# Optimization experiments

Hardware: AMD Instinct MI355X
Metric: run time of the kernel (lower is better)

## Reference

```python
import jax, jax.numpy as jnp
import numpy as np

K = 128           # top-k
NUM_SAMPLES = 500 # perturbation samples
SIGMA = 0.05      # noise scale (forward arg sigma in the torch module)


def setup_inputs() -> dict:
    key = jax.random.key(0)
    k1, k2 = jax.random.split(key)
    x = jax.random.normal(k1, (32, 2048), dtype=jnp.float32)
    noise = jax.random.normal(k2, (32, NUM_SAMPLES, 2048), dtype=jnp.float32)
    return {"x": x, "noise": noise}


def reference(x, noise):
    # x: (b, d) scores; noise: (b, n, d) standard-normal perturbations.
    b, d = x.shape
    n = noise.shape[1]
    perturbed = x[:, None, :] + noise * SIGMA          # (b, n, d)
    _, idx = jax.lax.top_k(perturbed, K)               # (b, n, K) indices into d
    idx = jnp.sort(idx, axis=-1)                       # sorted, matching torch.sort
    # indicators[b,j,d] = mean_n one_hot(idx[b,n,j], d)
    # Computed with a scatter-add instead of materializing the (b,n,K,d) one-hot.
    bi = jnp.arange(b)[:, None, None]                  # (b,1,1)
    ki = jnp.arange(K)[None, None, :]                  # (1,1,K)
    counts = jnp.zeros((b, K, d), dtype=x.dtype).at[bi, ki, idx].add(1.0)
    indicators = counts / n                            # (b, K, d)
    return indicators, idx
```

## Files before the change

### kernel.cpp

```cpp
#include <hip/hip_runtime.h>


constexpr int B_     = 32;
constexpr int D_     = 2048;
constexpr int NS_    = 500;
constexpr int TOPK_  = 128;
constexpr int SLACK_ = 32;
constexpr float SIGMA_  = 0.05f;
constexpr int PER_LANE_ = D_ / 64;
constexpr int HALF_  = D_ / 2;
constexpr int HPL_   = HALF_ / 64;
constexpr int CAP_   = 256;
constexpr int SLOTS_ = CAP_ / 64;
constexpr int JCHUNK_ = 8;

__device__ __forceinline__ uint32_t order_key(float f) {
  uint32_t u = __float_as_uint(f);
  return (u & 0x80000000u) ? ~u : (u | 0x80000000u);
}
__device__ __forceinline__ float inv_key(uint32_t k) {
  uint32_t u = (k & 0x80000000u) ? (k & 0x7FFFFFFFu) : ~k;
  return __uint_as_float(u);
}

__global__ __launch_bounds__(64) void ptk_cutoff(const float* __restrict__ x,
                                                 float* __restrict__ cutf) {
  const int lane = threadIdx.x & 63;
  const int b = blockIdx.x;
  const float* __restrict__ xr = x + (size_t)b * D_;
  uint32_t keys[PER_LANE_];
#pragma unroll
  for (int j = 0; j < PER_LANE_; j += 4) {
    const float4 xv = *reinterpret_cast<const float4*>(xr + lane * PER_LANE_ + j);
    keys[j + 0] = order_key(xv.x); keys[j + 1] = order_key(xv.y);
    keys[j + 2] = order_key(xv.z); keys[j + 3] = order_key(xv.w);
  }
  uint32_t prefix = 0; int k = TOPK_ + SLACK_;
#pragma unroll 1
  for (int bit = 31; bit >= 0; --bit) {
    const uint32_t want = (prefix >> bit) | 1u;
    int c = 0;
#pragma unroll
    for (int j = 0; j < PER_LANE_; ++j) c += ((keys[j] >> bit) == want) ? 1 : 0;
#pragma unroll
    for (int off = 32; off >= 1; off >>= 1) c += __shfl_xor(c, off);
    if (c >= k) prefix |= (1u << bit); else k -= c;
  }
  if (lane == 0) cutf[b] = inv_key(prefix);
}

__global__ __launch_bounds__(256) void ptk_select(
    const float* __restrict__ x, const float* __restrict__ noise,
    const float* __restrict__ cutf, float* __restrict__ out_idx) {
  __shared__ uint2 comp[2][2 * CAP_];
  __shared__ int cnts[2][2];

  const int lane = threadIdx.x & 63;
  const int wave = threadIdx.x >> 6;
  const int pair = wave >> 1;
  const int half = wave & 1;
  const int row  = blockIdx.x * 2 + pair;
  const int b = row / NS_;

  const float* __restrict__ xr = x + (size_t)b * D_ + half * HALF_;
  const float* __restrict__ nr = noise + (size_t)row * D_ + half * HALF_;
  const int base_l = lane * HPL_;
  const int base_i = half * HALF_ + base_l;

  float p[HPL_];
#pragma unroll
  for (int j = 0; j < HPL_; j += 4) {
    const float4 nv = *reinterpret_cast<const float4*>(nr + base_l + j);
    const float4 xv = *reinterpret_cast<const float4*>(xr + base_l + j);
    p[j + 0] = fmaf(SIGMA_, nv.x, xv.x);
    p[j + 1] = fmaf(SIGMA_, nv.y, xv.y);
    p[j + 2] = fmaf(SIGMA_, nv.z, xv.z);
    p[j + 3] = fmaf(SIGMA_, nv.w, xv.w);
  }

  const float cf = cutf[b];

  uint32_t m = 0;
#pragma unroll
  for (int j = 0; j < HPL_; ++j) m |= (p[j] >= cf) ? (1u << j) : 0u;
  const int cnt = __popc(m);

  const uint64_t below = (lane == 0) ? 0ull : ((~0ull) >> (64 - lane));
  int offset = 0, Cw = 0;
#pragma unroll
  for (int t = 0; t < 5; ++t) {
    const uint64_t mb = __ballot((cnt >> t) & 1);
    offset += (int)__popcll(mb & below) << t;
    Cw     += (int)__popcll(mb) << t;
  }
  if (lane == 0) cnts[pair][half] = Cw;

  {
    uint32_t mm = m; int q = half * CAP_ + offset;
    while (mm) {
      const int j = __ffs(mm) - 1; mm &= mm - 1;
      comp[pair][q] = make_uint2(order_key(p[j]), (uint32_t)(base_i + j));
      ++q;
    }
  }
  __syncthreads();

  if (half) return;

  const int C0 = cnts[pair][0];
  const int C1 = cnts[pair][1];
  const int C  = C0 + C1;

  float* __restrict__ idx_row = out_idx + (size_t)row * TOPK_;

  if (C >= TOPK_ && C <= CAP_) {
    uint32_t kk[SLOTS_], ki[SLOTS_];
    bool valid[SLOTS_];
#pragma unroll
    for (int s = 0; s < SLOTS_; ++s) {
      const int q = (s << 6) + lane;
      const int a = (q < C0) ? q : (CAP_ + q - C0);
      valid[s] = (q < C);
      const uint2 v = valid[s] ? comp[pair][a] : make_uint2(0u, 0u);
      kk[s] = v.x; ki[s] = v.y;
    }

    uint32_t orv = 0u, andv = 0xFFFFFFFFu;
#pragma unroll
    for (int s = 0; s < SLOTS_; ++s) {
      orv  |= valid[s] ? kk[s] : 0u;
      andv &= valid[s] ? kk[s] : 0xFFFFFFFFu;
    }
#pragma unroll
    for (int off = 32; off >= 1; off >>= 1) {
      orv  |= __shfl_xor(orv, off);
      andv &= __shfl_xor(andv, off);
    }
    const uint32_t diff = orv ^ andv;

    uint32_t prefix; int r;
    if (diff == 0u) {
      prefix = orv; r = TOPK_;
    } else {
      const int startbit = 31 - __clz(diff);
      prefix = (startbit == 31) ? 0u : (andv & (0xFFFFFFFFu << (startbit + 1)));
      int k = TOPK_;
      int A = C;
#pragma unroll 1
      for (int bit = startbit; bit >= 0; --bit) {
        const uint32_t want = (prefix >> bit) | 1u;
        int c = 0;
#pragma unroll
        for (int s = 0; s < SLOTS_; ++s)
          c += __popcll(__ballot((kk[s] >> bit) == want));
        if (c >= k) { prefix |= (1u << bit); A = c; }
        else        { k -= c; A -= c; }
        if (A == 1) {
          uint32_t mykey = 0u; bool have = false;
#pragma unroll
          for (int s = 0; s < SLOTS_; ++s) {
            const bool hit = valid[s] && ((kk[s] >> bit) == (prefix >> bit));
            mykey = hit ? kk[s] : mykey;
            have |= hit;
          }
          const uint64_t mb = __ballot(have);
          const int src = __ffsll((unsigned long long)mb) - 1;
          prefix = __shfl(mykey, src);
          k = 1;
          break;
        }
      }
      r = k;
    }

    int sel_run = 0, eq_run = 0;
#pragma unroll
    for (int s = 0; s < SLOTS_; ++s) {
      const bool gt = kk[s] > prefix;
      const bool eq = kk[s] == prefix;
      const uint64_t meq = __ballot(eq);
      const int eqrank = eq_run + __popcll(meq & below);
      const bool sel = gt || (eq && (eqrank < r));
      const uint64_t msel = __ballot(sel);
      if (sel) {
        const int pos = sel_run + __popcll(msel & below);
        idx_row[pos] = (float)(int)ki[s];
      }
      sel_run += __popcll(msel);
      eq_run  += __popcll(meq);
    }
  } else {
    const float* __restrict__ xr2 = x + (size_t)b * D_;
    const float* __restrict__ nr2 = noise + (size_t)row * D_;
    const int bi = lane * PER_LANE_;
    uint32_t keys[PER_LANE_];
#pragma unroll
    for (int j = 0; j < PER_LANE_; ++j)
      keys[j] = order_key(fmaf(SIGMA_, nr2[bi + j], xr2[bi + j]));

    uint32_t prefix = 0; int k = TOPK_;
#pragma unroll 1
    for (int bit = 31; bit >= 0; --bit) {
      const uint32_t want = (prefix >> bit) | 1u;
      int c = 0;
#pragma unroll
      for (int j = 0; j < PER_LANE_; ++j) c += ((keys[j] >> bit) == want) ? 1 : 0;
#pragma unroll
      for (int off = 32; off >= 1; off >>= 1) c += __shfl_xor(c, off);
      if (c >= k) prefix |= (1u << bit); else k -= c;
    }
    const int r = k;

    int gt = 0, eq = 0;
#pragma unroll
    for (int j = 0; j < PER_LANE_; ++j) {
      gt += (keys[j] > prefix) ? 1 : 0;
      eq += (keys[j] == prefix) ? 1 : 0;
    }
    uint32_t incl2 = (uint32_t)gt | ((uint32_t)eq << 16);
#pragma unroll
    for (int off = 1; off < 64; off <<= 1) {
      uint32_t y = __shfl_up(incl2, (unsigned)off);
      if (lane >= off) incl2 += y;
    }
    const int gt_base = (int)(incl2 & 0xFFFFu) - gt;
    const int eq_base = (int)(incl2 >> 16) - eq;
    int pos = gt_base + min(eq_base, r);
    int eq_seen = eq_base;
#pragma unroll
    for (int j = 0; j < PER_LANE_; ++j) {
      const uint32_t kj = keys[j];
      bool s = false;
      if (kj > prefix) s = true;
      else if (kj == prefix) { s = (eq_seen < r); eq_seen++; }
      if (s) { idx_row[pos] = (float)(bi + j); pos++; }
    }
  }
}

__global__ __launch_bounds__(256) void ptk_hist(
    const float* __restrict__ out_idx, float* __restrict__ indicators) {
  __shared__ int hist[JCHUNK_][D_];

  const int tid   = threadIdx.x;
  const int b     = blockIdx.x >> 4;
  const int chunk = blockIdx.x & 15;
  const int j0    = chunk * JCHUNK_;

  int4* h4 = (int4*)hist;
  for (int t = tid; t < JCHUNK_ * D_ / 4; t += 256)
    h4[t] = make_int4(0, 0, 0, 0);
  __syncthreads();

  const float* __restrict__ src = out_idx + (size_t)b * NS_ * TOPK_ + j0;
  for (int t = tid; t < NS_ * 2; t += 256) {
    const int n = t >> 1;
    const int q = (t & 1) << 2;
    const float4 v = *reinterpret_cast<const float4*>(src + (size_t)n * TOPK_ + q);
    atomicAdd(&hist[q + 0][(int)v.x], 1);
    atomicAdd(&hist[q + 1][(int)v.y], 1);
    atomicAdd(&hist[q + 2][(int)v.z], 1);
    atomicAdd(&hist[q + 3][(int)v.w], 1);
  }
  __syncthreads();

  float4* __restrict__ dst =
      (float4*)(indicators + ((size_t)b * TOPK_ + j0) * D_);
  for (int t = tid; t < JCHUNK_ * D_ / 4; t += 256) {
    const int4 h = h4[t];
    float4 o;
    o.x = (float)h.x / (float)NS_;
    o.y = (float)h.y / (float)NS_;
    o.z = (float)h.z / (float)NS_;
    o.w = (float)h.w / (float)NS_;
    dst[t] = o;
  }
}

extern "C" void kernel_launch(void* const* d_in, const int* in_sizes, int n_in,
                              void* d_out, int out_size, void* d_ws, size_t ws_size,
                              hipStream_t stream) {
  const float* x     = (const float*)d_in[0];
  const float* noise = (const float*)d_in[1];
  float* indicators  = (float*)d_out;
  float* out_idx     = (float*)d_out + (size_t)B_ * TOPK_ * D_;
  float* cutf        = (float*)d_ws;

  hipLaunchKernelGGL(ptk_cutoff, dim3(B_), dim3(64), 0, stream, x, cutf);

  const int rows = B_ * NS_;
  hipLaunchKernelGGL(ptk_select, dim3(rows / 2), dim3(256), 0, stream,
                     x, noise, cutf, out_idx);

  hipLaunchKernelGGL(ptk_hist, dim3(B_ * 16), dim3(256), 0, stream,
                     out_idx, indicators);
}
```

Baseline: 223.4 us.

## Defer fallback rows to a separate kernel and specialize finish by candidate count

Rows whose candidate count falls outside the fast window are no longer handled inline by a single wave doing a full 32-bit radix select. They are appended to a global list with an atomic and processed by a new small fallback kernel, which removes divergent slow paths from the main select kernel. The finish step is templated on the number of 64-wide slots needed (2, 3 or 4), so rows with fewer candidates do less ballot work. Other changes: the cutoff radix search stops at bit 14, giving a coarser threshold; the compaction loop is fully unrolled; and launch bounds request higher occupancy. The cost is an extra kernel launch plus a global atomic counter and list kept in workspace.

```diff
diff --git a/kernel.cpp b/kernel.cpp
--- a/kernel.cpp
+++ b/kernel.cpp
@@ -11,8 +11,8 @@
 constexpr int HALF_  = D_ / 2;
 constexpr int HPL_   = HALF_ / 64;
 constexpr int CAP_   = 256;
-constexpr int SLOTS_ = CAP_ / 64;
 constexpr int JCHUNK_ = 8;
+constexpr int CUTBIT_END_ = 14;
 
 __device__ __forceinline__ uint32_t order_key(float f) {
   uint32_t u = __float_as_uint(f);
@@ -24,7 +24,9 @@
 }
 
 __global__ __launch_bounds__(64) void ptk_cutoff(const float* __restrict__ x,
-                                                 float* __restrict__ cutf) {
+                                                 float* __restrict__ cutf,
+                                                 int* __restrict__ fb_cnt) {
+  if (blockIdx.x == 0 && threadIdx.x == 0) fb_cnt[0] = 0;
   const int lane = threadIdx.x & 63;
   const int b = blockIdx.x;
   const float* __restrict__ xr = x + (size_t)b * D_;
@@ -37,7 +39,7 @@
   }
   uint32_t prefix = 0; int k = TOPK_ + SLACK_;
 #pragma unroll 1
-  for (int bit = 31; bit >= 0; --bit) {
+  for (int bit = 31; bit >= CUTBIT_END_; --bit) {
     const uint32_t want = (prefix >> bit) | 1u;
     int c = 0;
 #pragma unroll
@@ -49,9 +51,92 @@
   if (lane == 0) cutf[b] = inv_key(prefix);
 }
 
-__global__ __launch_bounds__(256) void ptk_select(
+template <int NSLOT>
+__device__ __forceinline__ void finish_row(const uint2* __restrict__ comp,
+                                           const int C0, const int C,
+                                           float* __restrict__ idx_row,
+                                           const int lane, const uint64_t below) {
+  uint32_t kk[NSLOT], ki[NSLOT];
+#pragma unroll
+  for (int s = 0; s < NSLOT; ++s) {
+    const int q = (s << 6) + lane;
+    const int a = (q < C0) ? q : (CAP_ + q - C0);
+    const uint2 v = (q < C) ? comp[a] : make_uint2(0u, 0u);
+    kk[s] = v.x; ki[s] = v.y;
+  }
+
+  uint32_t orv = 0u, andv = 0xFFFFFFFFu;
+#pragma unroll
+  for (int s = 0; s < NSLOT; ++s) {
+    const bool valid = ((s << 6) + lane) < C;
+    orv  |= valid ? kk[s] : 0u;
+    andv &= valid ? kk[s] : 0xFFFFFFFFu;
+  }
+#pragma unroll
+  for (int off = 32; off >= 1; off >>= 1) {
+    orv  |= __shfl_xor(orv, off);
+    andv &= __shfl_xor(andv, off);
+  }
+  const uint32_t diff = orv ^ andv;
+
+  uint32_t prefix; int r;
+  if (diff == 0u) {
+    prefix = orv; r = TOPK_;
+  } else {
+    const int startbit = 31 - __clz(diff);
+    prefix = (startbit == 31) ? 0u : (andv & (0xFFFFFFFFu << (startbit + 1)));
+    int k = TOPK_;
+    int A = C;
+#pragma unroll 1
+    for (int bit = startbit; bit >= 0; --bit) {
+      const uint32_t want = (prefix >> bit) | 1u;
+      int c = 0;
+#pragma unroll
+      for (int s = 0; s < NSLOT; ++s)
+        c += __popcll(__ballot((kk[s] >> bit) == want));
+      if (c >= k) { prefix |= (1u << bit); A = c; }
+      else        { k -= c; A -= c; }
+      if (A == 1) {
+        uint32_t mykey = 0u; bool have = false;
+#pragma unroll
+        for (int s = 0; s < NSLOT; ++s) {
+          const bool valid = ((s << 6) + lane) < C;
+          const bool hit = valid && ((kk[s] >> bit) == (prefix >> bit));
+          mykey = hit ? kk[s] : mykey;
+          have |= hit;
+        }
+        const uint64_t mb = __ballot(have);
+        const int src = __ffsll((unsigned long long)mb) - 1;
+        prefix = __shfl(mykey, src);
+        k = 1;
+        break;
+      }
+    }
+    r = k;
+  }
+
+  int sel_run = 0, eq_run = 0;
+#pragma unroll
+  for (int s = 0; s < NSLOT; ++s) {
+    const bool gt = kk[s] > prefix;
+    const bool eq = kk[s] == prefix;
+    const uint64_t meq = __ballot(eq);
+    const int eqrank = eq_run + __popcll(meq & below);
+    const bool sel = gt || (eq && (eqrank < r));
+    const uint64_t msel = __ballot(sel);
+    if (sel) {
+      const int pos = sel_run + __popcll(msel & below);
+      idx_row[pos] = (float)(int)ki[s];
+    }
+    sel_run += __popcll(msel);
+    eq_run  += __popcll(meq);
+  }
+}
+
+__global__ __launch_bounds__(256, 8) void ptk_select(
     const float* __restrict__ x, const float* __restrict__ noise,
-    const float* __restrict__ cutf, float* __restrict__ out_idx) {
+    const float* __restrict__ cutf, float* __restrict__ out_idx,
+    int* __restrict__ fb_cnt, int* __restrict__ fb_list) {
   __shared__ uint2 comp[2][2 * CAP_];
   __shared__ int cnts[2][2];
 
@@ -96,11 +181,13 @@
   if (lane == 0) cnts[pair][half] = Cw;
 
   {
-    uint32_t mm = m; int q = half * CAP_ + offset;
-    while (mm) {
-      const int j = __ffs(mm) - 1; mm &= mm - 1;
-      comp[pair][q] = make_uint2(order_key(p[j]), (uint32_t)(base_i + j));
-      ++q;
+    int q = half * CAP_ + offset;
+#pragma unroll
+    for (int j = 0; j < HPL_; ++j) {
+      if (m & (1u << j)) {
+        comp[pair][q] = make_uint2(order_key(p[j]), (uint32_t)(base_i + j));
+        ++q;
+      }
     }
   }
   __syncthreads();
@@ -114,89 +201,36 @@
   float* __restrict__ idx_row = out_idx + (size_t)row * TOPK_;
 
   if (C >= TOPK_ && C <= CAP_) {
-    uint32_t kk[SLOTS_], ki[SLOTS_];
-    bool valid[SLOTS_];
-#pragma unroll
-    for (int s = 0; s < SLOTS_; ++s) {
-      const int q = (s << 6) + lane;
-      const int a = (q < C0) ? q : (CAP_ + q - C0);
-      valid[s] = (q < C);
-      const uint2 v = valid[s] ? comp[pair][a] : make_uint2(0u, 0u);
-      kk[s] = v.x; ki[s] = v.y;
-    }
-
-    uint32_t orv = 0u, andv = 0xFFFFFFFFu;
-#pragma unroll
-    for (int s = 0; s < SLOTS_; ++s) {
-      orv  |= valid[s] ? kk[s] : 0u;
-      andv &= valid[s] ? kk[s] : 0xFFFFFFFFu;
-    }
-#pragma unroll
-    for (int off = 32; off >= 1; off >>= 1) {
-      orv  |= __shfl_xor(orv, off);
-      andv &= __shfl_xor(andv, off);
-    }
-    const uint32_t diff = orv ^ andv;
-
-    uint32_t prefix; int r;
-    if (diff == 0u) {
-      prefix = orv; r = TOPK_;
-    } else {
-      const int startbit = 31 - __clz(diff);
-      prefix = (startbit == 31) ? 0u : (andv & (0xFFFFFFFFu << (startbit + 1)));
-      int k = TOPK_;
-      int A = C;
-#pragma unroll 1
-      for (int bit = startbit; bit >= 0; --bit) {
-        const uint32_t want = (prefix >> bit) | 1u;
-        int c = 0;
-#pragma unroll
-        for (int s = 0; s < SLOTS_; ++s)
-          c += __popcll(__ballot((kk[s] >> bit) == want));
-        if (c >= k) { prefix |= (1u << bit); A = c; }
-        else        { k -= c; A -= c; }
-        if (A == 1) {
-          uint32_t mykey = 0u; bool have = false;
-#pragma unroll
-          for (int s = 0; s < SLOTS_; ++s) {
-            const bool hit = valid[s] && ((kk[s] >> bit) == (prefix >> bit));
-            mykey = hit ? kk[s] : mykey;
-            have |= hit;
-          }
-          const uint64_t mb = __ballot(have);
-          const int src = __ffsll((unsigned long long)mb) - 1;
-          prefix = __shfl(mykey, src);
-          k = 1;
-          break;
-        }
-      }
-      r = k;
-    }
-
-    int sel_run = 0, eq_run = 0;
-#pragma unroll
-    for (int s = 0; s < SLOTS_; ++s) {
-      const bool gt = kk[s] > prefix;
-      const bool eq = kk[s] == prefix;
-      const uint64_t meq = __ballot(eq);
-      const int eqrank = eq_run + __popcll(meq & below);
-      const bool sel = gt || (eq && (eqrank < r));
-      const uint64_t msel = __ballot(sel);
-      if (sel) {
-        const int pos = sel_run + __popcll(msel & below);
-        idx_row[pos] = (float)(int)ki[s];
-      }
-      sel_run += __popcll(msel);
-      eq_run  += __popcll(meq);
-    }
+    const uint2* cp = comp[pair];
+    if (C <= 128)       finish_row<2>(cp, C0, C, idx_row, lane, below);
+    else if (C <= 192)  finish_row<3>(cp, C0, C, idx_row, lane, below);
+    else                finish_row<4>(cp, C0, C, idx_row, lane, below);
   } else {
-    const float* __restrict__ xr2 = x + (size_t)b * D_;
-    const float* __restrict__ nr2 = noise + (size_t)row * D_;
+    if (lane == 0) {
+      const int p_ = atomicAdd(fb_cnt, 1);
+      fb_list[p_] = row;
+    }
+  }
+}
+
+__global__ __launch_bounds__(64) void ptk_fb(
+    const float* __restrict__ x, const float* __restrict__ noise,
+    const int* __restrict__ fb_cnt, const int* __restrict__ fb_list,
+    float* __restrict__ out_idx) {
+  const int lane = threadIdx.x & 63;
+  const int cnt = fb_cnt[0];
+  for (int i = blockIdx.x; i < cnt; i += (int)gridDim.x) {
+    const int row = fb_list[i];
+    const int b = row / NS_;
+    const float* __restrict__ xr = x + (size_t)b * D_;
+    const float* __restrict__ nr = noise + (size_t)row * D_;
+    float* __restrict__ idx_row = out_idx + (size_t)row * TOPK_;
+
     const int bi = lane * PER_LANE_;
     uint32_t keys[PER_LANE_];
 #pragma unroll
     for (int j = 0; j < PER_LANE_; ++j)
-      keys[j] = order_key(fmaf(SIGMA_, nr2[bi + j], xr2[bi + j]));
+      keys[j] = order_key(fmaf(SIGMA_, nr[bi + j], xr[bi + j]));
 
     uint32_t prefix = 0; int k = TOPK_;
 #pragma unroll 1
@@ -285,12 +319,17 @@
   float* indicators  = (float*)d_out;
   float* out_idx     = (float*)d_out + (size_t)B_ * TOPK_ * D_;
   float* cutf        = (float*)d_ws;
-
-  hipLaunchKernelGGL(ptk_cutoff, dim3(B_), dim3(64), 0, stream, x, cutf);
+  int*   fb_cnt      = (int*)d_ws + 64;
+  int*   fb_list     = (int*)d_ws + 128;
+
+  hipLaunchKernelGGL(ptk_cutoff, dim3(B_), dim3(64), 0, stream, x, cutf, fb_cnt);
 
   const int rows = B_ * NS_;
   hipLaunchKernelGGL(ptk_select, dim3(rows / 2), dim3(256), 0, stream,
-                     x, noise, cutf, out_idx);
+                     x, noise, cutf, out_idx, fb_cnt, fb_list);
+
+  hipLaunchKernelGGL(ptk_fb, dim3(64), dim3(64), 0, stream,
+                     x, noise, fb_cnt, fb_list, out_idx);
 
   hipLaunchKernelGGL(ptk_hist, dim3(B_ * 16), dim3(256), 0, stream,
                      out_idx, indicators);
```

New measurement: 224.3 us. About the same (+0.4%).
